# Kernel tuning notes

Measured on AMD Instinct MI355X. Metric: run time of the kernel, lower is better.

Reference implementation:

```python
import jax, jax.numpy as jnp
import numpy as np

INPUT_DIM, HIDDEN_DIM, N_HEADS, N_AGENTS = 256, 512, 8, 64
BATCH, N_ENTITIES = 128, 256


def setup_inputs() -> dict:
    key = jax.random.key(0)
    ks = jax.random.split(key, 6)
    x = jax.random.normal(ks[0], (BATCH, N_ENTITIES, INPUT_DIM), dtype=jnp.float32)
    # encode: LeakyReLU -> Linear(input_dim, hidden_dim)
    W_enc = jax.random.normal(ks[1], (INPUT_DIM, HIDDEN_DIM), dtype=jnp.float32) * (1.0 / np.sqrt(INPUT_DIM))
    b_enc = jnp.zeros((HIDDEN_DIM,), dtype=jnp.float32)
    # per-head full hidden x hidden projections, stacked on head axis
    WQ = jax.random.normal(ks[2], (N_HEADS, HIDDEN_DIM, HIDDEN_DIM), dtype=jnp.float32)
    WK = jax.random.normal(ks[3], (N_HEADS, HIDDEN_DIM, HIDDEN_DIM), dtype=jnp.float32)
    WV = jax.random.normal(ks[4], (N_HEADS, HIDDEN_DIM, HIDDEN_DIM), dtype=jnp.float32)
    return {"x": x, "W_enc": W_enc, "b_enc": b_enc, "WQ": WQ, "WK": WK, "WV": WV, "n_agents": N_AGENTS}


def reference(x, W_enc, b_enc, WQ, WK, WV, n_agents):
    scale = 1.0 / np.sqrt(WQ.shape[-1]).astype(np.float32)
    # encode: LeakyReLU(0.01) then Linear
    h = jax.nn.leaky_relu(x, negative_slope=0.01) @ W_enc + b_enc  # [b, e, H]
    ha = h[:, :n_agents]  # [b, a, H]
    # all heads at once: n = head axis
    Q = jnp.einsum('bah,nhd->nbad', ha, WQ)
    K = jnp.einsum('beh,nhd->nbed', h, WK)
    V = jnp.einsum('beh,nhd->nbed', h, WV)
    scores = jnp.einsum('nbad,nbed->nbae', Q, K) * scale
    p = jax.nn.softmax(scores, axis=-1)
    # redundant renormalization from the original code
    prob = p / (jnp.sum(p, axis=-1, keepdims=True) + 1e-12)
    z = jnp.einsum('nbae,nbed->nbad', prob, V)  # [n, b, a, H]
    return jnp.mean(z, axis=0)  # [b, a, H]
```

## Files before the change

kernel.cpp:

```cpp
#include <hip/hip_runtime.h>
#include <math.h>

#define BATCH  128
#define NENT   256
#define INDIM  256
#define HID    512
#define NHEAD  8
#define NAGENT 64
#define SCALE  0.04419417382415922f


typedef unsigned short u16;
typedef unsigned int   u32;

typedef __bf16 bf16x8  __attribute__((ext_vector_type(8)));
typedef float  floatx4 __attribute__((ext_vector_type(4)));
typedef u32    u32x4   __attribute__((ext_vector_type(4)));
typedef u32    u32x2   __attribute__((ext_vector_type(2)));

union Frag {
    u32x4 s;
    struct { u32x2 lo, hi; } p;
    bf16x8 v;
};

__device__ __forceinline__ u16 f2bf(float x) {
    u32 u = __float_as_uint(x);
    return (u16)((u + 0x7FFFu + ((u >> 16) & 1u)) >> 16);
}
__device__ __forceinline__ float bf2f(u16 b) {
    return __uint_as_float(((u32)b) << 16);
}
__device__ __forceinline__ void split4(const float4& r, ushort4& hh, ushort4& hl) {
    hh.x = f2bf(r.x); hl.x = f2bf(r.x - bf2f(hh.x));
    hh.y = f2bf(r.y); hl.y = f2bf(r.y - bf2f(hh.y));
    hh.z = f2bf(r.z); hl.z = f2bf(r.z - bf2f(hh.z));
    hh.w = f2bf(r.w); hl.w = f2bf(r.w - bf2f(hh.w));
}

__global__ __launch_bounds__(256) void wenc_t_kernel(const float* __restrict__ W,
                                                     u16* __restrict__ Wt_p) {
    __shared__ float tile[64][68];
    const int bid = blockIdx.x;
    const int k0 = (bid & 3) * 64;
    const int d0 = (bid >> 2) * 64;
    const int t = threadIdx.x;
    const int ki = t >> 2, dc = (t & 3) * 16;
    #pragma unroll
    for (int c = 0; c < 4; ++c)
        *(float4*)&tile[ki][dc + c * 4] =
            *(const float4*)(W + (size_t)(k0 + ki) * HID + d0 + dc + c * 4);
    __syncthreads();
    const int dr = t >> 2, kc = (t & 3) * 16;
    #pragma unroll
    for (int c = 0; c < 4; ++c) {
        float4 v = make_float4(tile[kc + c * 4 + 0][dr], tile[kc + c * 4 + 1][dr],
                               tile[kc + c * 4 + 2][dr], tile[kc + c * 4 + 3][dr]);
        ushort4 hh, hl; split4(v, hh, hl);
        const int kk = k0 + kc + c * 4;
        size_t o = (size_t)(d0 + dr) * 512 + (size_t)(kk >> 5) * 64 + (kk & 31);
        *(ushort4*)(Wt_p + o) = hh;
        *(ushort4*)(Wt_p + o + 32) = hl;
    }
}

__global__ __launch_bounds__(256) void enc_kernel(const float* __restrict__ x,
                                                  const u16* __restrict__ Wt_p,
                                                  const float* __restrict__ bias,
                                                  u16* __restrict__ h_p) {
    __shared__ u16 Ah[32][264];
    __shared__ u16 Al[32][264];
    const int r0 = blockIdx.x * 32;
    const int t  = threadIdx.x;
    {
        const int row = t >> 3;
        const float* xr = x + (size_t)(r0 + row) * INDIM;
        #pragma unroll
        for (int j = 0; j < 8; ++j) {
            const int k0 = ((t & 7) + j * 8) * 4;
            float4 v = *(const float4*)(xr + k0);
            v.x = v.x > 0.f ? v.x : 0.01f * v.x;
            v.y = v.y > 0.f ? v.y : 0.01f * v.y;
            v.z = v.z > 0.f ? v.z : 0.01f * v.z;
            v.w = v.w > 0.f ? v.w : 0.01f * v.w;
            ushort4 hh, hl; split4(v, hh, hl);
            *(ushort4*)&Ah[row][k0] = hh;
            *(ushort4*)&Al[row][k0] = hl;
        }
    }
    __syncthreads();

    const int wid = t >> 6, lane = t & 63, l15 = lane & 15, quad = lane >> 4;
    const int mbase = (wid & 1) * 16;
    const int nbase = (wid >> 1) * 256;
    const floatx4 z4 = {0.f, 0.f, 0.f, 0.f};
    floatx4 acc[16];
    #pragma unroll
    for (int i = 0; i < 16; ++i) acc[i] = z4;

    for (int ks = 0; ks < 8; ++ks) {
        const int k = ks * 32 + quad * 8;
        Frag Afh, Afl;
        Afh.s = *(const u32x4*)&Ah[mbase + l15][k];
        Afl.s = *(const u32x4*)&Al[mbase + l15][k];
        #pragma unroll
        for (int nt = 0; nt < 16; ++nt) {
            const int d = nbase + nt * 16 + l15;
            const size_t wo = (size_t)d * 512 + (size_t)ks * 64 + quad * 8;
            Frag Bh, Bl;
            Bh.s = *(const u32x4*)(Wt_p + wo);
            Bl.s = *(const u32x4*)(Wt_p + wo + 32);
            floatx4 c = acc[nt];
            c = __builtin_amdgcn_mfma_f32_16x16x32_bf16(Afh.v, Bh.v, c, 0, 0, 0);
            c = __builtin_amdgcn_mfma_f32_16x16x32_bf16(Afh.v, Bl.v, c, 0, 0, 0);
            c = __builtin_amdgcn_mfma_f32_16x16x32_bf16(Afl.v, Bh.v, c, 0, 0, 0);
            acc[nt] = c;
        }
    }
    #pragma unroll
    for (int nt = 0; nt < 16; ++nt) {
        const int d = nbase + nt * 16 + l15;
        const float bv = bias[d];
        #pragma unroll
        for (int r = 0; r < 4; ++r) {
            const float v = acc[nt][r] + bv;
            const u16 hi = f2bf(v);
            const u16 lo = f2bf(v - bf2f(hi));
            const size_t o = (size_t)(r0 + mbase + quad * 4 + r) * 1024
                           + (size_t)(d >> 5) * 64 + (d & 31);
            h_p[o]      = hi;
            h_p[o + 32] = lo;
        }
    }
}

__global__ __launch_bounds__(256) void ht_kernel(const u16* __restrict__ h_p,
                                                 u16* __restrict__ hT) {
    __shared__ u16 tile[64][72];
    const int bid = blockIdx.x;
    const int dt = bid & 7;
    const int et = (bid >> 3) & 3;
    const int b  = bid >> 5;
    const int t  = threadIdx.x;
    const int r  = t >> 2, cs = (t & 3) * 16;
    const int dg = dt * 64 + cs;
    const u16* src = h_p + (size_t)(b * 256 + et * 64 + r) * 1024
                   + (size_t)(dg >> 5) * 64 + (dg & 31);
    *(ushort4*)&tile[r][cs + 0]  = *(const ushort4*)(src + 0);
    *(ushort4*)&tile[r][cs + 4]  = *(const ushort4*)(src + 4);
    *(ushort4*)&tile[r][cs + 8]  = *(const ushort4*)(src + 8);
    *(ushort4*)&tile[r][cs + 12] = *(const ushort4*)(src + 12);
    __syncthreads();
    const int d = t >> 2, es = (t & 3) * 16;
    u16* dst = hT + (size_t)b * 131072 + (size_t)(dt * 64 + d) * 256 + et * 64 + es;
    #pragma unroll
    for (int c = 0; c < 4; ++c) {
        ushort4 v = make_ushort4(tile[es + c * 4 + 0][d], tile[es + c * 4 + 1][d],
                                 tile[es + c * 4 + 2][d], tile[es + c * 4 + 3][d]);
        *(ushort4*)(dst + c * 4) = v;
    }
}

__global__ __launch_bounds__(256) void wqk_kernel(const float* __restrict__ WQ,
                                                  const float* __restrict__ WK,
                                                  u16* __restrict__ Mt_p) {
    __shared__ u16 Ah[64][72], Al[64][72], Bh[64][72], Bl[64][72];
    const int bid = blockIdx.x;
    const int jt = (bid & 7) * 64;
    const int it = ((bid >> 3) & 7) * 64;
    const int n  = bid >> 6;
    const float* qp = WQ + (size_t)n * 262144;
    const float* kp = WK + (size_t)n * 262144;
    const int t = threadIdx.x;
    const int wid = t >> 6, lane = t & 63, l15 = lane & 15, quad = lane >> 4;
    const int srow = t >> 2, sc = (t & 3) * 16;

    const floatx4 z4 = {0.f, 0.f, 0.f, 0.f};
    floatx4 acc[4];
    #pragma unroll
    for (int i = 0; i < 4; ++i) acc[i] = z4;

    for (int kc = 0; kc < HID; kc += 64) {
        #pragma unroll
        for (int f = 0; f < 4; ++f) {
            float4 va = *(const float4*)(kp + (size_t)(jt + srow) * HID + kc + sc + f * 4);
            ushort4 hh, hl; split4(va, hh, hl);
            *(ushort4*)&Ah[srow][sc + f * 4] = hh;
            *(ushort4*)&Al[srow][sc + f * 4] = hl;
            float4 vb = *(const float4*)(qp + (size_t)(it + srow) * HID + kc + sc + f * 4);
            split4(vb, hh, hl);
            *(ushort4*)&Bh[srow][sc + f * 4] = hh;
            *(ushort4*)&Bl[srow][sc + f * 4] = hl;
        }
        __syncthreads();
        #pragma unroll
        for (int ks = 0; ks < 2; ++ks) {
            const int k = ks * 32 + quad * 8;
            Frag Afh, Afl;
            Afh.s = *(const u32x4*)&Ah[wid * 16 + l15][k];
            Afl.s = *(const u32x4*)&Al[wid * 16 + l15][k];
            #pragma unroll
            for (int nt = 0; nt < 4; ++nt) {
                Frag Bfh, Bfl;
                Bfh.s = *(const u32x4*)&Bh[nt * 16 + l15][k];
                Bfl.s = *(const u32x4*)&Bl[nt * 16 + l15][k];
                floatx4 c = acc[nt];
                c = __builtin_amdgcn_mfma_f32_16x16x32_bf16(Afh.v, Bfh.v, c, 0, 0, 0);
                c = __builtin_amdgcn_mfma_f32_16x16x32_bf16(Afh.v, Bfl.v, c, 0, 0, 0);
                c = __builtin_amdgcn_mfma_f32_16x16x32_bf16(Afl.v, Bfh.v, c, 0, 0, 0);
                acc[nt] = c;
            }
        }
        __syncthreads();
    }
    #pragma unroll
    for (int nt = 0; nt < 4; ++nt)
        #pragma unroll
        for (int r = 0; r < 4; ++r) {
            const float v = acc[nt][r] * SCALE;
            const u16 hi = f2bf(v);
            const u16 lo = f2bf(v - bf2f(hi));
            const int j = jt + wid * 16 + quad * 4 + r;
            const int i = it + nt * 16 + l15;
            const size_t o = (size_t)n * 524288 + (size_t)j * 1024
                           + (size_t)(i >> 5) * 64 + (i & 31);
            Mt_p[o]      = hi;
            Mt_p[o + 32] = lo;
        }
}

__global__ __launch_bounds__(256) void wvt_kernel(const float* __restrict__ WV,
                                                  u16* __restrict__ WVt) {
    __shared__ float tile[64][68];
    const int bid = blockIdx.x;
    const int i0 = (bid & 7) * 64;
    const int o0 = ((bid >> 3) & 7) * 64;
    const int n  = bid >> 6;
    const float* src = WV + (size_t)n * 262144;
    const int t  = threadIdx.x;
    const int di = t >> 2;
    const int dc = (t & 3) * 16;
    #pragma unroll
    for (int c = 0; c < 4; ++c)
        *(float4*)&tile[di][dc + c * 4] =
            *(const float4*)(src + (size_t)(i0 + di) * HID + o0 + dc + c * 4);
    __syncthreads();
    const int dr = t >> 2;
    const int ic = (t & 3) * 16;
    size_t o = (size_t)n * 262144 + (size_t)(o0 + dr) * HID + i0 + ic;
    #pragma unroll
    for (int c = 0; c < 4; ++c) {
        ushort4 v = make_ushort4(f2bf(tile[ic + c * 4 + 0][dr]), f2bf(tile[ic + c * 4 + 1][dr]),
                                 f2bf(tile[ic + c * 4 + 2][dr]), f2bf(tile[ic + c * 4 + 3][dr]));
        *(ushort4*)(WVt + o + c * 4) = v;
    }
}

template<bool USE_HT>
__global__ __launch_bounds__(256, 3) void attn_kernel(const u16* __restrict__ h_p,
                                                      const u16* __restrict__ Mt_p,
                                                      const u16* __restrict__ WVt,
                                                      const u16* __restrict__ hT,
                                                      float* __restrict__ out) {
    __shared__ __align__(16) char SM[53504];
    u16*   Th  = (u16*)SM;
    u16*   Tl  = (u16*)(SM + 16640);
    float* S   = (float*)SM;
    float* red = (float*)(SM + 33792);
    u16*   HbT = (u16*)SM;
    u16*   U   = (u16*)SM;
    u16*   Pt  = (u16*)(SM + 36864);

    const int bid = blockIdx.x;
    const int x7 = bid & 7;
    const int s  = bid >> 3;
    const int at = s & 1;
    const int n  = (x7 >> 1) | (((s >> 1) & 1) << 2);
    const int b  = ((s >> 2) << 1) | (x7 & 1);

    const int tid  = threadIdx.x;
    const int wid  = tid >> 6;
    const int lane = tid & 63;
    const int l15  = lane & 15;
    const int quad = lane >> 4;

    const u16* Mtp = Mt_p + (size_t)n * 524288;
    const u16* Wv  = WVt  + (size_t)n * 262144;
    const u16* hTb = hT + (size_t)b * 131072;
    const size_t hb_base = (size_t)b * 262144;
    const size_t ha_row0 = hb_base + (size_t)(at * 32) * 1024;

    const floatx4 z4 = {0.f, 0.f, 0.f, 0.f};
    floatx4 Sacc[8];
    #pragma unroll
    for (int i = 0; i < 8; ++i) Sacc[i] = z4;

    for (int H = 0; H < 2; ++H) {
        floatx4 Tacc[8];
        #pragma unroll
        for (int i = 0; i < 8; ++i) Tacc[i] = z4;
        for (int ks = 0; ks < 16; ++ks) {
            const int ko = ks * 64 + quad * 8;
            Frag Ahf[2], Alf[2];
            #pragma unroll
            for (int mt = 0; mt < 2; ++mt) {
                const size_t ro = ha_row0 + (size_t)(mt * 16 + l15) * 1024 + ko;
                Ahf[mt].s = *(const u32x4*)(h_p + ro);
                Alf[mt].s = *(const u32x4*)(h_p + ro + 32);
            }
            #pragma unroll
            for (int nt = 0; nt < 4; ++nt) {
                const int d = H * 256 + (wid * 4 + nt) * 16 + l15;
                const size_t mo = (size_t)d * 1024 + ko;
                Frag Bh, Bl;
                Bh.s = *(const u32x4*)(Mtp + mo);
                Bl.s = *(const u32x4*)(Mtp + mo + 32);
                #pragma unroll
                for (int mt = 0; mt < 2; ++mt) {
                    floatx4 c = Tacc[mt * 4 + nt];
                    c = __builtin_amdgcn_mfma_f32_16x16x32_bf16(Ahf[mt].v, Bh.v, c, 0, 0, 0);
                    c = __builtin_amdgcn_mfma_f32_16x16x32_bf16(Ahf[mt].v, Bl.v, c, 0, 0, 0);
                    c = __builtin_amdgcn_mfma_f32_16x16x32_bf16(Alf[mt].v, Bh.v, c, 0, 0, 0);
                    Tacc[mt * 4 + nt] = c;
                }
            }
        }
        __syncthreads();
        #pragma unroll
        for (int mt = 0; mt < 2; ++mt)
            #pragma unroll
            for (int nt = 0; nt < 4; ++nt)
                #pragma unroll
                for (int r = 0; r < 4; ++r) {
                    const float v = Tacc[mt * 4 + nt][r];
                    const int a  = mt * 16 + quad * 4 + r;
                    const int dl = (wid * 4 + nt) * 16 + l15;
                    const u16 hi = f2bf(v);
                    Th[a * 260 + dl] = hi;
                    Tl[a * 260 + dl] = f2bf(v - bf2f(hi));
                }
        __syncthreads();
        for (int ks = 0; ks < 8; ++ks) {
            const int kl = ks * 32 + quad * 8;
            const int ko = (H * 8 + ks) * 64 + quad * 8;
            Frag Ahf[4], Alf[4];
            #pragma unroll
            for (int mt = 0; mt < 4; ++mt) {
                const size_t ro = hb_base + (size_t)((wid * 4 + mt) * 16 + l15) * 1024 + ko;
                Ahf[mt].s = *(const u32x4*)(h_p + ro);
                Alf[mt].s = *(const u32x4*)(h_p + ro + 32);
            }
            #pragma unroll
            for (int nt = 0; nt < 2; ++nt) {
                const int ac = nt * 16 + l15;
                Frag Bfh, Bfl;
                Bfh.p.lo = *(const u32x2*)(Th + ac * 260 + kl);
                Bfh.p.hi = *(const u32x2*)(Th + ac * 260 + kl + 4);
                Bfl.p.lo = *(const u32x2*)(Tl + ac * 260 + kl);
                Bfl.p.hi = *(const u32x2*)(Tl + ac * 260 + kl + 4);
                #pragma unroll
                for (int mt = 0; mt < 4; ++mt) {
                    floatx4 c = Sacc[mt * 2 + nt];
                    c = __builtin_amdgcn_mfma_f32_16x16x32_bf16(Ahf[mt].v, Bfh.v, c, 0, 0, 0);
                    c = __builtin_amdgcn_mfma_f32_16x16x32_bf16(Ahf[mt].v, Bfl.v, c, 0, 0, 0);
                    c = __builtin_amdgcn_mfma_f32_16x16x32_bf16(Alf[mt].v, Bfh.v, c, 0, 0, 0);
                    Sacc[mt * 2 + nt] = c;
                }
            }
        }
    }
    __syncthreads();
    #pragma unroll
    for (int mt = 0; mt < 4; ++mt)
        #pragma unroll
        for (int nt = 0; nt < 2; ++nt)
            #pragma unroll
            for (int r = 0; r < 4; ++r) {
                const int e = (wid * 4 + mt) * 16 + quad * 4 + r;
                const int a = nt * 16 + l15;
                S[e * 33 + a] = Sacc[mt * 2 + nt][r];
            }
    __syncthreads();
    {
        const int a   = tid & 31;
        const int seg = tid >> 5;
        float v[32];
        #pragma unroll
        for (int i = 0; i < 32; ++i) v[i] = S[(seg * 32 + i) * 33 + a];
        float mx = v[0];
        #pragma unroll
        for (int i = 1; i < 32; ++i) mx = fmaxf(mx, v[i]);
        red[a * 8 + seg] = mx;
        __syncthreads();
        float gmx = red[a * 8 + 0];
        #pragma unroll
        for (int i = 1; i < 8; ++i) gmx = fmaxf(gmx, red[a * 8 + i]);
        __syncthreads();
        float sum = 0.f;
        #pragma unroll
        for (int i = 0; i < 32; ++i) { v[i] = expf(v[i] - gmx); sum += v[i]; }
        red[a * 8 + seg] = sum;
        __syncthreads();
        float tot = 0.f;
        #pragma unroll
        for (int i = 0; i < 8; ++i) tot += red[a * 8 + i];
        const float inv = 1.0f / tot;
        #pragma unroll
        for (int i = 0; i < 32; ++i)
            Pt[a * 260 + seg * 32 + i] = f2bf(v[i] * inv);
    }
    __syncthreads();
    floatx4 Uacc[16];
    #pragma unroll
    for (int i = 0; i < 16; ++i) Uacc[i] = z4;
    const int d0w = wid * 128;
    if (USE_HT) {
        for (int ep = 0; ep < 4; ++ep) {
            Frag Bc[2][8];
            #pragma unroll
            for (int sb = 0; sb < 2; ++sb)
                #pragma unroll
                for (int dt = 0; dt < 8; ++dt) {
                    const int d = d0w + dt * 16 + l15;
                    Bc[sb][dt].s = *(const u32x4*)(hTb + (size_t)d * 256
                                                   + (2 * ep + sb) * 32 + quad * 8);
                }
            #pragma unroll
            for (int sb = 0; sb < 2; ++sb) {
                const int et = 2 * ep + sb;
                Frag Ap[2];
                #pragma unroll
                for (int mt = 0; mt < 2; ++mt) {
                    const int ar = mt * 16 + l15;
                    Ap[mt].p.lo = *(const u32x2*)(Pt + ar * 260 + et * 32 + quad * 8);
                    Ap[mt].p.hi = *(const u32x2*)(Pt + ar * 260 + et * 32 + quad * 8 + 4);
                }
                #pragma unroll
                for (int dt = 0; dt < 8; ++dt)
                    #pragma unroll
                    for (int mt = 0; mt < 2; ++mt)
                        Uacc[mt * 8 + dt] = __builtin_amdgcn_mfma_f32_16x16x32_bf16(
                            Ap[mt].v, Bc[sb][dt].v, Uacc[mt * 8 + dt], 0, 0, 0);
            }
        }
    } else {
        u32* Hb32 = (u32*)HbT;
        for (int et = 0; et < 8; ++et) {
            {
                const int epi = lane & 15;
                const int q   = lane >> 4;
                const size_t r0p = hb_base + (size_t)(et * 32 + 2 * epi) * 1024;
                #pragma unroll
                for (int c = 0; c < 4; ++c) {
                    const int d0 = d0w + c * 32 + q * 8;
                    const size_t po = (size_t)(d0 >> 5) * 64 + (d0 & 31);
                    u32x4 u0 = *(const u32x4*)(h_p + r0p + po);
                    u32x4 u1 = *(const u32x4*)(h_p + r0p + 1024 + po);
                    #pragma unroll
                    for (int p = 0; p < 4; ++p) {
                        const u32 w0 = (u0[p] & 0xFFFFu) | (u1[p] << 16);
                        const u32 w1 = (u0[p] >> 16) | (u1[p] & 0xFFFF0000u);
                        Hb32[(d0 + 2 * p) * 18 + epi]     = w0;
                        Hb32[(d0 + 2 * p + 1) * 18 + epi] = w1;
                    }
                }
            }
            Frag Ap[2];
            #pragma unroll
            for (int mt = 0; mt < 2; ++mt) {
                const int ar = mt * 16 + l15;
                Ap[mt].p.lo = *(const u32x2*)(Pt + ar * 260 + et * 32 + quad * 8);
                Ap[mt].p.hi = *(const u32x2*)(Pt + ar * 260 + et * 32 + quad * 8 + 4);
            }
            #pragma unroll
            for (int dt = 0; dt < 8; ++dt) {
                const int d = d0w + dt * 16 + l15;
                Frag Bf;
                Bf.p.lo = *(const u32x2*)(HbT + d * 36 + quad * 8);
                Bf.p.hi = *(const u32x2*)(HbT + d * 36 + quad * 8 + 4);
                #pragma unroll
                for (int mt = 0; mt < 2; ++mt)
                    Uacc[mt * 8 + dt] = __builtin_amdgcn_mfma_f32_16x16x32_bf16(
                        Ap[mt].v, Bf.v, Uacc[mt * 8 + dt], 0, 0, 0);
            }
        }
    }
    __syncthreads();
    #pragma unroll
    for (int mt = 0; mt < 2; ++mt)
        #pragma unroll
        for (int dt = 0; dt < 8; ++dt)
            #pragma unroll
            for (int r = 0; r < 4; ++r) {
                const int a = mt * 16 + quad * 4 + r;
                const int d = d0w + dt * 16 + l15;
                U[a * 520 + d] = f2bf(Uacc[mt * 8 + dt][r]);
            }
    __syncthreads();
    floatx4 Zacc[16];
    #pragma unroll
    for (int i = 0; i < 16; ++i) Zacc[i] = z4;
    for (int kp = 0; kp < 8; ++kp) {
        Frag Bw[2][8];
        #pragma unroll
        for (int sb = 0; sb < 2; ++sb) {
            const int k = (kp * 2 + sb) * 32 + quad * 8;
            #pragma unroll
            for (int dt = 0; dt < 8; ++dt) {
                const int dn = (wid * 8 + dt) * 16 + l15;
                Bw[sb][dt].s = *(const u32x4*)(Wv + (size_t)dn * HID + k);
            }
        }
        #pragma unroll
        for (int sb = 0; sb < 2; ++sb) {
            const int k = (kp * 2 + sb) * 32 + quad * 8;
            Frag Au[2];
            #pragma unroll
            for (int mt = 0; mt < 2; ++mt) {
                Au[mt].p.lo = *(const u32x2*)(U + (mt * 16 + l15) * 520 + k);
                Au[mt].p.hi = *(const u32x2*)(U + (mt * 16 + l15) * 520 + k + 4);
            }
            #pragma unroll
            for (int dt = 0; dt < 8; ++dt)
                #pragma unroll
                for (int mt = 0; mt < 2; ++mt)
                    Zacc[mt * 8 + dt] = __builtin_amdgcn_mfma_f32_16x16x32_bf16(
                        Au[mt].v, Bw[sb][dt].v, Zacc[mt * 8 + dt], 0, 0, 0);
        }
    }
    float* ob = out + ((size_t)b * NAGENT + at * 32) * HID;
    #pragma unroll
    for (int mt = 0; mt < 2; ++mt)
        #pragma unroll
        for (int dt = 0; dt < 8; ++dt)
            #pragma unroll
            for (int r = 0; r < 4; ++r) {
                const int a  = mt * 16 + quad * 4 + r;
                const int dn = (wid * 8 + dt) * 16 + l15;
                atomicAdd(ob + (size_t)a * HID + dn, Zacc[mt * 8 + dt][r] * 0.125f);
            }
}

extern "C" void kernel_launch(void* const* d_in, const int* in_sizes, int n_in,
                              void* d_out, int out_size, void* d_ws, size_t ws_size,
                              hipStream_t stream) {
    const float* x     = (const float*)d_in[0];
    const float* W_enc = (const float*)d_in[1];
    const float* b_enc = (const float*)d_in[2];
    const float* WQ    = (const float*)d_in[3];
    const float* WK    = (const float*)d_in[4];
    const float* WV    = (const float*)d_in[5];
    float* out = (float*)d_out;

    char* ws = (char*)d_ws;
    u16* h_p  = (u16*)ws;
    u16* Mt_p = (u16*)(ws + 67108864);
    u16* WVt  = (u16*)(ws + 75497472);
    u16* hT   = (u16*)(ws + 79691776);
    u16* Wt_p = WVt;

    const bool useHT = ws_size >= (size_t)113246208;

    hipMemsetAsync(d_out, 0, (size_t)out_size * sizeof(float), stream);
    wenc_t_kernel<<<32, 256, 0, stream>>>(W_enc, Wt_p);
    enc_kernel<<<1024, 256, 0, stream>>>(x, Wt_p, b_enc, h_p);
    if (useHT) ht_kernel<<<4096, 256, 0, stream>>>(h_p, hT);
    wvt_kernel<<<512, 256, 0, stream>>>(WV, WVt);
    wqk_kernel<<<512, 256, 0, stream>>>(WQ, WK, Mt_p);
    if (useHT)
        attn_kernel<true><<<2048, 256, 0, stream>>>(h_p, Mt_p, WVt, hT, out);
    else
        attn_kernel<false><<<2048, 256, 0, stream>>>(h_p, Mt_p, WVt, hT, out);
}
```

Baseline: 975.8 us.

## Compute softmax in MFMA registers and shrink LDS for higher occupancy

The softmax now reduces directly on the score accumulators using lane shuffles and small per-wave partial arrays, replacing the round trip through an LDS score matrix. Without that matrix the USE_HT variant can drop its LDS allocation, so launch bounds rise from 3 to 4 blocks per SM. The block-to-(head, batch, agent-tile) mapping also changes to a plain linear order, which alters L2 locality. It also swaps expf for __expf, with small accuracy risk, and the higher occupancy target may pressure registers or cause spills.

```diff
diff --git a/kernel.cpp b/kernel.cpp
--- a/kernel.cpp
+++ b/kernel.cpp
@@ -257,26 +257,26 @@
 }
 
 template<bool USE_HT>
-__global__ __launch_bounds__(256, 3) void attn_kernel(const u16* __restrict__ h_p,
+__global__ __launch_bounds__(256, 4) void attn_kernel(const u16* __restrict__ h_p,
                                                       const u16* __restrict__ Mt_p,
                                                       const u16* __restrict__ WVt,
                                                       const u16* __restrict__ hT,
                                                       float* __restrict__ out) {
-    __shared__ __align__(16) char SM[53504];
-    u16*   Th  = (u16*)SM;
-    u16*   Tl  = (u16*)(SM + 16640);
-    float* S   = (float*)SM;
-    float* red = (float*)(SM + 33792);
-    u16*   HbT = (u16*)SM;
-    u16*   U   = (u16*)SM;
-    u16*   Pt  = (u16*)(SM + 36864);
+    constexpr int SMSZ = USE_HT ? 34304 : 53504;
+    __shared__ __align__(16) char SM[SMSZ];
+    u16*   Th   = (u16*)SM;
+    u16*   Tl   = (u16*)(SM + 16640);
+    float* redm = (float*)(SM + 33280);
+    float* reds = (float*)(SM + 33792);
+    u16*   HbT  = (u16*)SM;
+    u16*   U    = (u16*)SM;
+    u16*   Pt   = (u16*)(SM + (USE_HT ? 0 : 36864));
 
     const int bid = blockIdx.x;
-    const int x7 = bid & 7;
-    const int s  = bid >> 3;
-    const int at = s & 1;
-    const int n  = (x7 >> 1) | (((s >> 1) & 1) << 2);
-    const int b  = ((s >> 2) << 1) | (x7 & 1);
+    const int n   = bid & 7;
+    const int idx = bid >> 3;
+    const int b   = idx >> 1;
+    const int at  = idx & 1;
 
     const int tid  = threadIdx.x;
     const int wid  = tid >> 6;
@@ -369,45 +369,64 @@
             }
         }
     }
-    __syncthreads();
-    #pragma unroll
-    for (int mt = 0; mt < 4; ++mt)
-        #pragma unroll
-        for (int nt = 0; nt < 2; ++nt)
-            #pragma unroll
-            for (int r = 0; r < 4; ++r) {
-                const int e = (wid * 4 + mt) * 16 + quad * 4 + r;
-                const int a = nt * 16 + l15;
-                S[e * 33 + a] = Sacc[mt * 2 + nt][r];
-            }
-    __syncthreads();
     {
-        const int a   = tid & 31;
-        const int seg = tid >> 5;
-        float v[32];
-        #pragma unroll
-        for (int i = 0; i < 32; ++i) v[i] = S[(seg * 32 + i) * 33 + a];
-        float mx = v[0];
-        #pragma unroll
-        for (int i = 1; i < 32; ++i) mx = fmaxf(mx, v[i]);
-        red[a * 8 + seg] = mx;
+        float mloc[2], sloc[2];
+        #pragma unroll
+        for (int nt = 0; nt < 2; ++nt) {
+            float m = Sacc[nt][0];
+            #pragma unroll
+            for (int mt = 0; mt < 4; ++mt)
+                #pragma unroll
+                for (int r = 0; r < 4; ++r)
+                    m = fmaxf(m, Sacc[mt * 2 + nt][r]);
+            m = fmaxf(m, __shfl_xor(m, 16, 64));
+            m = fmaxf(m, __shfl_xor(m, 32, 64));
+            mloc[nt] = m;
+        }
+        if (quad == 0) {
+            redm[wid * 32 + l15]      = mloc[0];
+            redm[wid * 32 + 16 + l15] = mloc[1];
+        }
         __syncthreads();
-        float gmx = red[a * 8 + 0];
-        #pragma unroll
-        for (int i = 1; i < 8; ++i) gmx = fmaxf(gmx, red[a * 8 + i]);
+        #pragma unroll
+        for (int nt = 0; nt < 2; ++nt) {
+            const int a = nt * 16 + l15;
+            const float g = fmaxf(fmaxf(redm[a], redm[32 + a]),
+                                  fmaxf(redm[64 + a], redm[96 + a]));
+            float s = 0.f;
+            #pragma unroll
+            for (int mt = 0; mt < 4; ++mt)
+                #pragma unroll
+                for (int r = 0; r < 4; ++r) {
+                    const float e = __expf(Sacc[mt * 2 + nt][r] - g);
+                    Sacc[mt * 2 + nt][r] = e;
+                    s += e;
+                }
+            s += __shfl_xor(s, 16, 64);
+            s += __shfl_xor(s, 32, 64);
+            sloc[nt] = s;
+        }
+        if (quad == 0) {
+            reds[wid * 32 + l15]      = sloc[0];
+            reds[wid * 32 + 16 + l15] = sloc[1];
+        }
         __syncthreads();
-        float sum = 0.f;
-        #pragma unroll
-        for (int i = 0; i < 32; ++i) { v[i] = expf(v[i] - gmx); sum += v[i]; }
-        red[a * 8 + seg] = sum;
-        __syncthreads();
-        float tot = 0.f;
-        #pragma unroll
-        for (int i = 0; i < 8; ++i) tot += red[a * 8 + i];
-        const float inv = 1.0f / tot;
-        #pragma unroll
-        for (int i = 0; i < 32; ++i)
-            Pt[a * 260 + seg * 32 + i] = f2bf(v[i] * inv);
+        #pragma unroll
+        for (int nt = 0; nt < 2; ++nt) {
+            const int a = nt * 16 + l15;
+            const float tot = reds[a] + reds[32 + a] + reds[64 + a] + reds[96 + a];
+            const float inv = 1.0f / tot;
+            #pragma unroll
+            for (int mt = 0; mt < 4; ++mt) {
+                ushort4 pv;
+                pv.x = f2bf(Sacc[mt * 2 + nt][0] * inv);
+                pv.y = f2bf(Sacc[mt * 2 + nt][1] * inv);
+                pv.z = f2bf(Sacc[mt * 2 + nt][2] * inv);
+                pv.w = f2bf(Sacc[mt * 2 + nt][3] * inv);
+                const int e0 = (wid * 4 + mt) * 16 + quad * 4;
+                *(ushort4*)(Pt + a * 260 + e0) = pv;
+            }
+        }
     }
     __syncthreads();
     floatx4 Uacc[16];
```

Result: slower. 1.152 ms (+18.0%).

## Merge agent-halves into 512-thread attention blocks sharing LDS-staged Mt tiles

Applied to the files above, without the earlier changes.

Replaces the 256-thread attention kernel (one block per 32-agent half) with a 512-thread kernel where both agent halves of a (head, batch) pair share a block. The Q·K-projection weight tiles and agent rows are staged cooperatively into LDS via global_load_lds, so each Mt tile is fetched once per block instead of once per half. This halves redundant global/L2 traffic for the largest weight operand, at the cost of extra block-wide barriers per k-step, larger LDS footprint and potentially lower occupancy. The non-hT fallback is kept as a separate kernel.

```diff
diff --git a/kernel.cpp b/kernel.cpp
--- a/kernel.cpp
+++ b/kernel.cpp
@@ -36,6 +36,14 @@
     hh.y = f2bf(r.y); hl.y = f2bf(r.y - bf2f(hh.y));
     hh.z = f2bf(r.z); hl.z = f2bf(r.z - bf2f(hh.z));
     hh.w = f2bf(r.w); hl.w = f2bf(r.w - bf2f(hh.w));
+}
+__device__ __forceinline__ floatx4 mm(const Frag& a, const Frag& b, floatx4 c) {
+    return __builtin_amdgcn_mfma_f32_16x16x32_bf16(a.v, b.v, c, 0, 0, 0);
+}
+__device__ __forceinline__ void gl16(const u16* g, char* l) {
+    __builtin_amdgcn_global_load_lds(
+        (const __attribute__((address_space(1))) u32*)g,
+        (__attribute__((address_space(3))) u32*)l, 16, 0, 0);
 }
 
 __global__ __launch_bounds__(256) void wenc_t_kernel(const float* __restrict__ W,
@@ -256,12 +264,264 @@
     }
 }
 
-template<bool USE_HT>
-__global__ __launch_bounds__(256, 3) void attn_kernel(const u16* __restrict__ h_p,
-                                                      const u16* __restrict__ Mt_p,
-                                                      const u16* __restrict__ WVt,
-                                                      const u16* __restrict__ hT,
-                                                      float* __restrict__ out) {
+__global__ __launch_bounds__(512, 4) void attn512_kernel(const u16* __restrict__ h_p,
+                                                         const u16* __restrict__ Mt_p,
+                                                         const u16* __restrict__ WVt,
+                                                         const u16* __restrict__ hT,
+                                                         float* __restrict__ out) {
+    __shared__ __align__(16) char SM[69632];
+
+    const int bid = blockIdx.x;
+    const int x7 = bid & 7;
+    const int s  = bid >> 3;
+    const int n  = (x7 >> 1) | ((s & 1) << 2);
+    const int b  = ((s >> 1) << 1) | (x7 & 1);
+
+    const int tid  = threadIdx.x;
+    const int wave = tid >> 6;
+    const int ath  = wave >> 2;
+    const int wl   = wave & 3;
+    const int lane = tid & 63;
+    const int l15  = lane & 15;
+    const int quad = lane >> 4;
+
+    const u16* Mtp = Mt_p + (size_t)n * 524288;
+    const u16* Wv  = WVt  + (size_t)n * 262144;
+    const u16* hTb = hT + (size_t)b * 131072;
+    const size_t hb_base = (size_t)b * 262144;
+
+    u16* Th_h = (u16*)(SM + ath * 33280);
+    u16* Tl_h = (u16*)(SM + ath * 33280 + 16640);
+
+    const floatx4 z4 = {0.f, 0.f, 0.f, 0.f};
+    floatx4 Sacc[8];
+    #pragma unroll
+    for (int i = 0; i < 8; ++i) Sacc[i] = z4;
+
+    for (int H = 0; H < 2; ++H) {
+        __syncthreads();
+        floatx4 Tacc[8];
+        #pragma unroll
+        for (int i = 0; i < 8; ++i) Tacc[i] = z4;
+        const int d0 = H * 256;
+        const u16* mtS = (const u16*)SM;
+        const u16* haS = (const u16*)(SM + 32768);
+        for (int ks = 0; ks < 16; ++ks) {
+            #pragma unroll
+            for (int j = 0; j < 4; ++j)
+                gl16(Mtp + (size_t)(d0 + j * 64 + lane) * 1024 + ks * 64 + wave * 8,
+                     SM + (wave * 4 + j) * 1024);
+            gl16(h_p + hb_base + (size_t)lane * 1024 + ks * 64 + wave * 8,
+                 SM + 32768 + wave * 1024);
+            __syncthreads();
+            Frag Ah0, Al0, Ah1, Al1;
+            const int R0 = ath * 32 + l15;
+            Ah0.s = *(const u32x4*)(haS + ((quad)     * 64 + R0)      * 8);
+            Al0.s = *(const u32x4*)(haS + ((4 + quad) * 64 + R0)      * 8);
+            Ah1.s = *(const u32x4*)(haS + ((quad)     * 64 + R0 + 16) * 8);
+            Al1.s = *(const u32x4*)(haS + ((4 + quad) * 64 + R0 + 16) * 8);
+            #pragma unroll
+            for (int nt = 0; nt < 4; ++nt) {
+                const int row = (wl * 4 + nt) * 16 + l15;
+                Frag Bh, Bl;
+                Bh.s = *(const u32x4*)(mtS + ((quad)     * 256 + row) * 8);
+                Bl.s = *(const u32x4*)(mtS + ((4 + quad) * 256 + row) * 8);
+                floatx4 c0 = Tacc[nt], c1 = Tacc[4 + nt];
+                c0 = mm(Ah0, Bh, c0); c0 = mm(Ah0, Bl, c0); c0 = mm(Al0, Bh, c0);
+                c1 = mm(Ah1, Bh, c1); c1 = mm(Ah1, Bl, c1); c1 = mm(Al1, Bh, c1);
+                Tacc[nt] = c0; Tacc[4 + nt] = c1;
+            }
+            __syncthreads();
+        }
+        #pragma unroll
+        for (int mt = 0; mt < 2; ++mt)
+            #pragma unroll
+            for (int nt = 0; nt < 4; ++nt)
+                #pragma unroll
+                for (int r = 0; r < 4; ++r) {
+                    const float v = Tacc[mt * 4 + nt][r];
+                    const int a  = mt * 16 + quad * 4 + r;
+                    const int dl = (wl * 4 + nt) * 16 + l15;
+                    const u16 hi = f2bf(v);
+                    Th_h[a * 260 + dl] = hi;
+                    Tl_h[a * 260 + dl] = f2bf(v - bf2f(hi));
+                }
+        __syncthreads();
+        for (int ks = 0; ks < 8; ++ks) {
+            const int kl = ks * 32 + quad * 8;
+            const int ko = (H * 8 + ks) * 64 + quad * 8;
+            #pragma unroll
+            for (int mtp = 0; mtp < 2; ++mtp) {
+                Frag Ahf[2], Alf[2];
+                #pragma unroll
+                for (int mt = 0; mt < 2; ++mt) {
+                    const int row = (wl * 4 + mtp * 2 + mt) * 16 + l15;
+                    const size_t ro = hb_base + (size_t)row * 1024 + ko;
+                    Ahf[mt].s = *(const u32x4*)(h_p + ro);
+                    Alf[mt].s = *(const u32x4*)(h_p + ro + 32);
+                }
+                #pragma unroll
+                for (int nt = 0; nt < 2; ++nt) {
+                    const int ac = nt * 16 + l15;
+                    Frag Bfh, Bfl;
+                    Bfh.p.lo = *(const u32x2*)(Th_h + ac * 260 + kl);
+                    Bfh.p.hi = *(const u32x2*)(Th_h + ac * 260 + kl + 4);
+                    Bfl.p.lo = *(const u32x2*)(Tl_h + ac * 260 + kl);
+                    Bfl.p.hi = *(const u32x2*)(Tl_h + ac * 260 + kl + 4);
+                    #pragma unroll
+                    for (int mt = 0; mt < 2; ++mt) {
+                        floatx4 c = Sacc[(mtp * 2 + mt) * 2 + nt];
+                        c = mm(Ahf[mt], Bfh, c);
+                        c = mm(Ahf[mt], Bfl, c);
+                        c = mm(Alf[mt], Bfh, c);
+                        Sacc[(mtp * 2 + mt) * 2 + nt] = c;
+                    }
+                }
+            }
+        }
+    }
+    __syncthreads();
+    {
+        float* S_h = (float*)(SM + ath * 33792);
+        #pragma unroll
+        for (int mt = 0; mt < 4; ++mt)
+            #pragma unroll
+            for (int nt = 0; nt < 2; ++nt)
+                #pragma unroll
+                for (int r = 0; r < 4; ++r) {
+                    const int e = (wl * 4 + mt) * 16 + quad * 4 + r;
+                    const int a = nt * 16 + l15;
+                    S_h[e * 33 + a] = Sacc[mt * 2 + nt][r];
+                }
+    }
+    __syncthreads();
+    {
+        const int h   = tid >> 8;
+        const int t8  = tid & 255;
+        const int a   = t8 & 31;
+        const int seg = t8 >> 5;
+        float* Sh   = (float*)(SM + h * 33792);
+        float* redh = (float*)(SM + 67584 + h * 1024);
+        u16*   Pth  = (u16*)(SM + h * 16640);
+        float v[32];
+        #pragma unroll
+        for (int i = 0; i < 32; ++i) v[i] = Sh[(seg * 32 + i) * 33 + a];
+        float mx = v[0];
+        #pragma unroll
+        for (int i = 1; i < 32; ++i) mx = fmaxf(mx, v[i]);
+        redh[a * 8 + seg] = mx;
+        __syncthreads();
+        float gmx = redh[a * 8 + 0];
+        #pragma unroll
+        for (int i = 1; i < 8; ++i) gmx = fmaxf(gmx, redh[a * 8 + i]);
+        __syncthreads();
+        float sum = 0.f;
+        #pragma unroll
+        for (int i = 0; i < 32; ++i) { v[i] = expf(v[i] - gmx); sum += v[i]; }
+        redh[a * 8 + seg] = sum;
+        __syncthreads();
+        float tot = 0.f;
+        #pragma unroll
+        for (int i = 0; i < 8; ++i) tot += redh[a * 8 + i];
+        const float inv = 1.0f / tot;
+        #pragma unroll
+        for (int i = 0; i < 32; ++i)
+            Pth[a * 260 + seg * 32 + i] = f2bf(v[i] * inv);
+    }
+    __syncthreads();
+    floatx4 Uacc[16];
+    #pragma unroll
+    for (int i = 0; i < 16; ++i) Uacc[i] = z4;
+    const int d0w = wl * 128;
+    {
+        const u16* Pt_h = (const u16*)(SM + ath * 16640);
+        for (int ep = 0; ep < 4; ++ep) {
+            #pragma unroll
+            for (int sb = 0; sb < 2; ++sb) {
+                const int et = 2 * ep + sb;
+                Frag Bc[8];
+                #pragma unroll
+                for (int dt = 0; dt < 8; ++dt) {
+                    const int d = d0w + dt * 16 + l15;
+                    Bc[dt].s = *(const u32x4*)(hTb + (size_t)d * 256
+                                               + et * 32 + quad * 8);
+                }
+                Frag Ap[2];
+                #pragma unroll
+                for (int mt = 0; mt < 2; ++mt) {
+                    const int ar = mt * 16 + l15;
+                    Ap[mt].p.lo = *(const u32x2*)(Pt_h + ar * 260 + et * 32 + quad * 8);
+                    Ap[mt].p.hi = *(const u32x2*)(Pt_h + ar * 260 + et * 32 + quad * 8 + 4);
+                }
+                #pragma unroll
+                for (int dt = 0; dt < 8; ++dt)
+                    #pragma unroll
+                    for (int mt = 0; mt < 2; ++mt)
+                        Uacc[mt * 8 + dt] = mm(Ap[mt], Bc[dt], Uacc[mt * 8 + dt]);
+            }
+        }
+    }
+    __syncthreads();
+    {
+        u16* U_h = (u16*)(SM + ath * 33280);
+        #pragma unroll
+        for (int mt = 0; mt < 2; ++mt)
+            #pragma unroll
+            for (int dt = 0; dt < 8; ++dt)
+                #pragma unroll
+                for (int r = 0; r < 4; ++r) {
+                    const int a = mt * 16 + quad * 4 + r;
+                    const int d = d0w + dt * 16 + l15;
+                    U_h[a * 520 + d] = f2bf(Uacc[mt * 8 + dt][r]);
+                }
+    }
+    __syncthreads();
+    floatx4 Zacc[16];
+    #pragma unroll
+    for (int i = 0; i < 16; ++i) Zacc[i] = z4;
+    {
+        const u16* U_h = (const u16*)(SM + ath * 33280);
+        for (int kp = 0; kp < 8; ++kp) {
+            #pragma unroll
+            for (int sb = 0; sb < 2; ++sb) {
+                const int k = (kp * 2 + sb) * 32 + quad * 8;
+                Frag Bw[8];
+                #pragma unroll
+                for (int dt = 0; dt < 8; ++dt) {
+                    const int dn = (wl * 8 + dt) * 16 + l15;
+                    Bw[dt].s = *(const u32x4*)(Wv + (size_t)dn * HID + k);
+                }
+                Frag Au[2];
+                #pragma unroll
+                for (int mt = 0; mt < 2; ++mt) {
+                    Au[mt].p.lo = *(const u32x2*)(U_h + (mt * 16 + l15) * 520 + k);
+                    Au[mt].p.hi = *(const u32x2*)(U_h + (mt * 16 + l15) * 520 + k + 4);
+                }
+                #pragma unroll
+                for (int dt = 0; dt < 8; ++dt)
+                    #pragma unroll
+                    for (int mt = 0; mt < 2; ++mt)
+                        Zacc[mt * 8 + dt] = mm(Au[mt], Bw[dt], Zacc[mt * 8 + dt]);
+            }
+        }
+    }
+    float* ob = out + ((size_t)b * NAGENT + ath * 32) * HID;
+    #pragma unroll
+    for (int mt = 0; mt < 2; ++mt)
+        #pragma unroll
+        for (int dt = 0; dt < 8; ++dt)
+            #pragma unroll
+            for (int r = 0; r < 4; ++r) {
+                const int a  = mt * 16 + quad * 4 + r;
+                const int dn = (wl * 8 + dt) * 16 + l15;
+                atomicAdd(ob + (size_t)a * HID + dn, Zacc[mt * 8 + dt][r] * 0.125f);
+            }
+}
+
+__global__ __launch_bounds__(256, 3) void attn_noht_kernel(const u16* __restrict__ h_p,
+                                                           const u16* __restrict__ Mt_p,
+                                                           const u16* __restrict__ WVt,
+                                                           float* __restrict__ out) {
     __shared__ __align__(16) char SM[53504];
     u16*   Th  = (u16*)SM;
     u16*   Tl  = (u16*)(SM + 16640);
@@ -286,7 +546,6 @@
 
     const u16* Mtp = Mt_p + (size_t)n * 524288;
     const u16* Wv  = WVt  + (size_t)n * 262144;
-    const u16* hTb = hT + (size_t)b * 131072;
     const size_t hb_base = (size_t)b * 262144;
     const size_t ha_row0 = hb_base + (size_t)(at * 32) * 1024;
 
@@ -318,9 +577,9 @@
                 #pragma unroll
                 for (int mt = 0; mt < 2; ++mt) {
                     floatx4 c = Tacc[mt * 4 + nt];
-                    c = __builtin_amdgcn_mfma_f32_16x16x32_bf16(Ahf[mt].v, Bh.v, c, 0, 0, 0);
-                    c = __builtin_amdgcn_mfma_f32_16x16x32_bf16(Ahf[mt].v, Bl.v, c, 0, 0, 0);
-                    c = __builtin_amdgcn_mfma_f32_16x16x32_bf16(Alf[mt].v, Bh.v, c, 0, 0, 0);
+                    c = mm(Ahf[mt], Bh, c);
+                    c = mm(Ahf[mt], Bl, c);
+                    c = mm(Alf[mt], Bh, c);
                     Tacc[mt * 4 + nt] = c;
                 }
             }
@@ -361,9 +620,9 @@
                 #pragma unroll
                 for (int mt = 0; mt < 4; ++mt) {
                     floatx4 c = Sacc[mt * 2 + nt];
-                    c = __builtin_amdgcn_mfma_f32_16x16x32_bf16(Ahf[mt].v, Bfh.v, c, 0, 0, 0);
-                    c = __builtin_amdgcn_mfma_f32_16x16x32_bf16(Ahf[mt].v, Bfl.v, c, 0, 0, 0);
-                    c = __builtin_amdgcn_mfma_f32_16x16x32_bf16(Alf[mt].v, Bfh.v, c, 0, 0, 0);
+                    c = mm(Ahf[mt], Bfh, c);
+                    c = mm(Ahf[mt], Bfl, c);
+                    c = mm(Alf[mt], Bfh, c);
                     Sacc[mt * 2 + nt] = c;
                 }
             }
@@ -414,36 +673,7 @@
     #pragma unroll
     for (int i = 0; i < 16; ++i) Uacc[i] = z4;
     const int d0w = wid * 128;
-    if (USE_HT) {
-        for (int ep = 0; ep < 4; ++ep) {
-            Frag Bc[2][8];
-            #pragma unroll
-            for (int sb = 0; sb < 2; ++sb)
-                #pragma unroll
-                for (int dt = 0; dt < 8; ++dt) {
-                    const int d = d0w + dt * 16 + l15;
-                    Bc[sb][dt].s = *(const u32x4*)(hTb + (size_t)d * 256
-                                                   + (2 * ep + sb) * 32 + quad * 8);
-                }
-            #pragma unroll
-            for (int sb = 0; sb < 2; ++sb) {
-                const int et = 2 * ep + sb;
-                Frag Ap[2];
-                #pragma unroll
-                for (int mt = 0; mt < 2; ++mt) {
-                    const int ar = mt * 16 + l15;
-                    Ap[mt].p.lo = *(const u32x2*)(Pt + ar * 260 + et * 32 + quad * 8);
-                    Ap[mt].p.hi = *(const u32x2*)(Pt + ar * 260 + et * 32 + quad * 8 + 4);
-                }
-                #pragma unroll
-                for (int dt = 0; dt < 8; ++dt)
-                    #pragma unroll
-                    for (int mt = 0; mt < 2; ++mt)
-                        Uacc[mt * 8 + dt] = __builtin_amdgcn_mfma_f32_16x16x32_bf16(
-                            Ap[mt].v, Bc[sb][dt].v, Uacc[mt * 8 + dt], 0, 0, 0);
-            }
-        }
-    } else {
+    {
         u32* Hb32 = (u32*)HbT;
         for (int et = 0; et < 8; ++et) {
             {
@@ -452,16 +682,16 @@
                 const size_t r0p = hb_base + (size_t)(et * 32 + 2 * epi) * 1024;
                 #pragma unroll
                 for (int c = 0; c < 4; ++c) {
-                    const int d0 = d0w + c * 32 + q * 8;
-                    const size_t po = (size_t)(d0 >> 5) * 64 + (d0 & 31);
+                    const int d0c = d0w + c * 32 + q * 8;
+                    const size_t po = (size_t)(d0c >> 5) * 64 + (d0c & 31);
                     u32x4 u0 = *(const u32x4*)(h_p + r0p + po);
                     u32x4 u1 = *(const u32x4*)(h_p + r0p + 1024 + po);
                     #pragma unroll
                     for (int p = 0; p < 4; ++p) {
                         const u32 w0 = (u0[p] & 0xFFFFu) | (u1[p] << 16);
                         const u32 w1 = (u0[p] >> 16) | (u1[p] & 0xFFFF0000u);
-                        Hb32[(d0 + 2 * p) * 18 + epi]     = w0;
-                        Hb32[(d0 + 2 * p + 1) * 18 + epi] = w1;
+                        Hb32[(d0c + 2 * p) * 18 + epi]     = w0;
+                        Hb32[(d0c + 2 * p + 1) * 18 + epi] = w1;
                     }
                 }
             }
@@ -480,8 +710,7 @@
                 Bf.p.hi = *(const u32x2*)(HbT + d * 36 + quad * 8 + 4);
                 #pragma unroll
                 for (int mt = 0; mt < 2; ++mt)
-                    Uacc[mt * 8 + dt] = __builtin_amdgcn_mfma_f32_16x16x32_bf16(
-                        Ap[mt].v, Bf.v, Uacc[mt * 8 + dt], 0, 0, 0);
+                    Uacc[mt * 8 + dt] = mm(Ap[mt], Bf, Uacc[mt * 8 + dt]);
             }
         }
     }
@@ -524,8 +753,7 @@
             for (int dt = 0; dt < 8; ++dt)
                 #pragma unroll
                 for (int mt = 0; mt < 2; ++mt)
-                    Zacc[mt * 8 + dt] = __builtin_amdgcn_mfma_f32_16x16x32_bf16(
-                        Au[mt].v, Bw[sb][dt].v, Zacc[mt * 8 + dt], 0, 0, 0);
+                    Zacc[mt * 8 + dt] = mm(Au[mt], Bw[sb][dt], Zacc[mt * 8 + dt]);
         }
     }
     float* ob = out + ((size_t)b * NAGENT + at * 32) * HID;
@@ -568,7 +796,7 @@
     wvt_kernel<<<512, 256, 0, stream>>>(WV, WVt);
     wqk_kernel<<<512, 256, 0, stream>>>(WQ, WK, Mt_p);
     if (useHT)
-        attn_kernel<true><<<2048, 256, 0, stream>>>(h_p, Mt_p, WVt, hT, out);
+        attn512_kernel<<<1024, 512, 0, stream>>>(h_p, Mt_p, WVt, hT, out);
     else
-        attn_kernel<false><<<2048, 256, 0, stream>>>(h_p, Mt_p, WVt, hT, out);
-}
+        attn_noht_kernel<<<2048, 256, 0, stream>>>(h_p, Mt_p, WVt, out);
+}
```

Result: faster. 812.6 us (-16.7%).
